# Optimization experiments

Measured on AMD Instinct MI355X. Metric: run time of the kernel, lower is better.

The kernel has to match this reference:

```python
import jax, jax.numpy as jnp
import numpy as np

B, L, D, H = 65536, 20, 4, 1024
T = 61  # output_length; 60 RK4 steps


def setup_inputs() -> dict:
    key = jax.random.key(0)
    ks = jax.random.split(key, 16)
    # small positive states so the quadratic SEIR dynamics stay finite over 60 steps
    xx = jax.random.uniform(ks[0], (B, L, D), dtype=jnp.float32) * 0.1
    dims = [L * D] + [H] * 6 + [3]
    inp = {"xx": xx}
    for i in range(7):
        scale = 1.0 / np.sqrt(dims[i])
        W = jax.random.normal(ks[1 + 2 * i], (dims[i], dims[i + 1]), dtype=jnp.float32) * scale
        if i == 6:
            W = W * 1e-3  # keep beta/gamma/sigma small -> stable integration
        inp[f"W{i}"] = W
        inp[f"b{i}"] = jnp.zeros((dims[i + 1],), jnp.float32)
    inp["output_length"] = T
    return inp


def reference(xx, W0, b0, W1, b1, W2, b2, W3, b3, W4, b4, W5, b5, W6, b6, output_length):
    h = xx.reshape(xx.shape[0], -1)  # (B, L*D)
    for W, b in ((W0, b0), (W1, b1), (W2, b2), (W3, b3), (W4, b4), (W5, b5)):
        h = jax.nn.leaky_relu(h @ W + b, negative_slope=0.01)
    out = h @ W6 + b6  # (B, 3)
    beta, gamma, sigma = out[:, 0:1], out[:, 1:2], out[:, 2:3]  # each (B,1)

    initial = xx[:, 0]  # (B, 4) = S,E,I,R at t0
    S0, E0, I0, R0 = (initial[:, i:i + 1] for i in range(4))
    # self.step = 1 in the torch module, so dt is folded in as 1.0

    def derivs(S, E, I):
        SI = beta * S * I
        return -SI, SI - sigma * E, sigma * E - gamma * I, gamma * I

    def body(carry, _):
        S, E, I, R = carry
        k1S, k1E, k1I, k1R = derivs(S, E, I)
        k2S, k2E, k2I, k2R = derivs(S + 0.5 * k1S, E + 0.5 * k1E, I + 0.5 * k1I)
        k3S, k3E, k3I, k3R = derivs(S + 0.5 * k2S, E + 0.5 * k2E, I + 0.5 * k2I)
        k4S, k4E, k4I, k4R = derivs(S + k3S, E + k3E, I + k3I)
        upd = lambda f, k1, k2, k3, k4: f + (k1 + 2 * k2 + 2 * k3 + k4) / 6.0
        new = (upd(S, k1S, k2S, k3S, k4S),
               upd(E, k1E, k2E, k3E, k4E),
               upd(I, k1I, k2I, k3I, k4I),
               upd(R, k1R, k2R, k3R, k4R))
        return new, jnp.concatenate(new, axis=1)  # (B,4) per step

    _, ys = jax.lax.scan(body, (S0, E0, I0, R0), None, length=output_length - 1)
    y0 = jnp.concatenate([S0, E0, I0, R0], axis=1)  # (B,4)
    y = jnp.concatenate([y0[None], ys], axis=0)     # (T,B,4)
    return jnp.transpose(y, (1, 0, 2))              # (B,T,4) in S,E,I,R order
```

## Files before the change

kernel.cpp:

```cpp
#include <hip/hip_runtime.h>
#include <stdint.h>

typedef short s16x8 __attribute__((ext_vector_type(8)));
typedef __bf16 bf16x8 __attribute__((ext_vector_type(8)));
typedef float f32x4 __attribute__((ext_vector_type(4)));

typedef const __attribute__((address_space(1))) void* gas_ptr;
typedef __attribute__((address_space(3))) void* las_ptr;

__device__ __forceinline__ unsigned short f2bf(float f) {
  unsigned u = __builtin_bit_cast(unsigned, f);
  u += 0x7FFFu + ((u >> 16) & 1u);
  return (unsigned short)(u >> 16);
}
__device__ __forceinline__ float bf2f(unsigned short h) {
  return __builtin_bit_cast(float, (unsigned)h << 16);
}

__device__ __forceinline__ void async16(const void* g, void* l) {
  __builtin_amdgcn_global_load_lds((gas_ptr)g, (las_ptr)l, 16, 0, 0);
}

__global__ void prep_x0(const float* __restrict__ xx, unsigned short* __restrict__ X0,
                        int rowOffset, int rows) {
  int idx = blockIdx.x * blockDim.x + threadIdx.x;
  if (idx >= rows * 128) return;
  int r = idx >> 7, c = idx & 127;
  float v = (c < 80) ? xx[(size_t)(rowOffset + r) * 80 + c] : 0.f;
  X0[(size_t)r * 128 + c] = f2bf(v);
}

__global__ void transpose_cast(const float* __restrict__ W, unsigned short* __restrict__ WT,
                               int K, int N, int KP) {
  __shared__ float tile[32][33];
  int n0 = blockIdx.x * 32, k0 = blockIdx.y * 32;
  int tx = threadIdx.x, ty = threadIdx.y;
  #pragma unroll
  for (int j = 0; j < 32; j += 8) {
    int k = k0 + ty + j;
    tile[ty + j][tx] = (k < K) ? W[(size_t)k * N + n0 + tx] : 0.f;
  }
  __syncthreads();
  #pragma unroll
  for (int j = 0; j < 32; j += 8) {
    WT[(size_t)(n0 + ty + j) * KP + k0 + tx] = f2bf(tile[tx][ty + j]);
  }
}

#define BM 128
#define BN 128
#define BK 64

__global__ void gemm_mlp(const unsigned short* __restrict__ A,
                         const unsigned short* __restrict__ BT,
                         const float* __restrict__ bias,
                         unsigned short* __restrict__ C,
                         int M, int N, int K, int leaky) {
  __shared__ unsigned short As[BM * BK];
  __shared__ unsigned short Bs[BN * BK];

  const int tid  = threadIdx.x;
  const int wid  = tid >> 6;
  const int lane = tid & 63;
  const int wr = (wid >> 1) * 64;
  const int wc = (wid & 1) * 64;
  const int bn = blockIdx.x * BN;
  const int bm = blockIdx.y * BM;

  const int srow = lane >> 3;
  const int scol = (lane & 7) * 8;

  f32x4 acc[4][4] = {};

  const unsigned short* aTile = A  + (size_t)bm * K;
  const unsigned short* bTile = BT + (size_t)bn * K;

  for (int k0 = 0; k0 < K; k0 += BK) {
    #pragma unroll
    for (int j = 0; j < 4; ++j) {
      const int rg = wid + j * 4;
      async16(aTile + (size_t)(rg * 8 + srow) * K + k0 + scol, &As[rg * 8 * BK]);
      async16(bTile + (size_t)(rg * 8 + srow) * K + k0 + scol, &Bs[rg * 8 * BK]);
    }
    __syncthreads();

    const int fr = lane & 15;
    const int kq = (lane >> 4) * 8;
    #pragma unroll
    for (int ks = 0; ks < BK; ks += 32) {
      const int kk = ks + kq;
      bf16x8 af[4], bv[4];
      #pragma unroll
      for (int m = 0; m < 4; ++m)
        af[m] = __builtin_bit_cast(bf16x8, *(const s16x8*)&As[(wr + m * 16 + fr) * BK + kk]);
      #pragma unroll
      for (int n = 0; n < 4; ++n)
        bv[n] = __builtin_bit_cast(bf16x8, *(const s16x8*)&Bs[(wc + n * 16 + fr) * BK + kk]);
      #pragma unroll
      for (int m = 0; m < 4; ++m)
        #pragma unroll
        for (int n = 0; n < 4; ++n)
          acc[m][n] = __builtin_amdgcn_mfma_f32_16x16x32_bf16(af[m], bv[n], acc[m][n], 0, 0, 0);
    }
    __syncthreads();
  }

  const int fcol = lane & 15;
  const int frow = (lane >> 4) * 4;
  #pragma unroll
  for (int m = 0; m < 4; ++m) {
    #pragma unroll
    for (int n = 0; n < 4; ++n) {
      const int col = bn + wc + n * 16 + fcol;
      const float bb = bias[col];
      #pragma unroll
      for (int r = 0; r < 4; ++r) {
        const int row = bm + wr + m * 16 + frow + r;
        float v = acc[m][n][r] + bb;
        if (leaky) v = (v > 0.f) ? v : 0.01f * v;
        C[(size_t)row * N + col] = f2bf(v);
      }
    }
  }
}

__global__ void head_gemv(const unsigned short* __restrict__ H,
                          const float* __restrict__ W6,
                          const float* __restrict__ b6,
                          float* __restrict__ bgs,
                          int rows) {
  const int w = (blockIdx.x * blockDim.x + threadIdx.x) >> 6;
  const int lane = threadIdx.x & 63;
  if (w >= rows) return;

  const unsigned short* h = H + (size_t)w * 1024 + lane * 16;
  float s0 = 0.f, s1 = 0.f, s2 = 0.f;
  #pragma unroll
  for (int i = 0; i < 16; i += 8) {
    s16x8 v = *(const s16x8*)(h + i);
    #pragma unroll
    for (int j = 0; j < 8; ++j) {
      const float hv = bf2f((unsigned short)v[j]);
      const int e = lane * 16 + i + j;
      s0 = fmaf(hv, W6[e * 3 + 0], s0);
      s1 = fmaf(hv, W6[e * 3 + 1], s1);
      s2 = fmaf(hv, W6[e * 3 + 2], s2);
    }
  }
  #pragma unroll
  for (int off = 1; off < 64; off <<= 1) {
    s0 += __shfl_xor(s0, off);
    s1 += __shfl_xor(s1, off);
    s2 += __shfl_xor(s2, off);
  }
  if (lane == 0) {
    float4 v = make_float4(s0 + b6[0], s1 + b6[1], s2 + b6[2], 0.f);
    *(float4*)(bgs + (size_t)w * 4) = v;
  }
}

__global__ void rk4_traj(const float* __restrict__ bgs,
                         const float* __restrict__ xx,
                         float* __restrict__ out,
                         int rowOffset, int rows, int T) {
  const int r = blockIdx.x * blockDim.x + threadIdx.x;
  if (r >= rows) return;
  const size_t grow = (size_t)rowOffset + r;

  const float4 bg = *(const float4*)(bgs + (size_t)r * 4);
  const float beta = bg.x, gamma = bg.y, sigma = bg.z;

  const float4 iv = *(const float4*)(xx + grow * 80);
  float S = iv.x, E = iv.y, I = iv.z, R = iv.w;
  float* o = out + grow * (size_t)T * 4;
  *(float4*)o = iv;

#define DERIVS(S_, E_, I_, dS, dE, dI, dR)      \
  {                                             \
    float SI = beta * (S_) * (I_);              \
    float sE = sigma * (E_);                    \
    float gI = gamma * (I_);                    \
    dS = -SI; dE = SI - sE; dI = sE - gI; dR = gI; \
  }

  for (int t = 1; t < T; ++t) {
    float k1S, k1E, k1I, k1R; DERIVS(S, E, I, k1S, k1E, k1I, k1R);
    float k2S, k2E, k2I, k2R; DERIVS(S + 0.5f * k1S, E + 0.5f * k1E, I + 0.5f * k1I, k2S, k2E, k2I, k2R);
    float k3S, k3E, k3I, k3R; DERIVS(S + 0.5f * k2S, E + 0.5f * k2E, I + 0.5f * k2I, k3S, k3E, k3I, k3R);
    float k4S, k4E, k4I, k4R; DERIVS(S + k3S, E + k3E, I + k3I, k4S, k4E, k4I, k4R);
    S += (k1S + 2.f * k2S + 2.f * k3S + k4S) * (1.f / 6.f);
    E += (k1E + 2.f * k2E + 2.f * k3E + k4E) * (1.f / 6.f);
    I += (k1I + 2.f * k2I + 2.f * k3I + k4I) * (1.f / 6.f);
    R += (k1R + 2.f * k2R + 2.f * k3R + k4R) * (1.f / 6.f);
    *(float4*)(o + (size_t)t * 4) = make_float4(S, E, I, R);
  }
#undef DERIVS
}

extern "C" void kernel_launch(void* const* d_in, const int* in_sizes, int n_in,
                              void* d_out, int out_size, void* d_ws, size_t ws_size,
                              hipStream_t stream) {
  const float* xx = (const float*)d_in[0];
  const float* W[7];
  const float* bb[7];
  for (int i = 0; i < 7; ++i) {
    W[i]  = (const float*)d_in[1 + 2 * i];
    bb[i] = (const float*)d_in[2 + 2 * i];
  }
  const int B = in_sizes[0] / 80;
  const int T = out_size / (B * 4);
  float* out = (float*)d_out;

  uint8_t* ws = (uint8_t*)d_ws;
  size_t off = 0;
  auto alloc = [&](size_t bytes) -> uint8_t* {
    uint8_t* p = ws + off;
    off += (bytes + 255) & ~(size_t)255;
    return p;
  };

  unsigned short* WTl[6];
  WTl[0] = (unsigned short*)alloc((size_t)1024 * 128 * 2);
  for (int i = 1; i < 6; ++i) WTl[i] = (unsigned short*)alloc((size_t)1024 * 1024 * 2);

  const size_t weightBytes = off;
  const size_t avail = ws_size > weightBytes ? ws_size - weightBytes : 0;
  int Bc = (int)(avail / 4368);
  Bc = (Bc / 128) * 128;
  if (Bc > B) Bc = B;
  if (Bc < 128) Bc = 128;

  unsigned short* X0   = (unsigned short*)alloc((size_t)Bc * 128 * 2);
  unsigned short* buf0 = (unsigned short*)alloc((size_t)Bc * 1024 * 2);
  unsigned short* buf1 = (unsigned short*)alloc((size_t)Bc * 1024 * 2);
  float* bgs           = (float*)alloc((size_t)Bc * 4 * 4);

  {
    dim3 blk(32, 8);
    transpose_cast<<<dim3(32, 4), blk, 0, stream>>>(W[0], WTl[0], 80, 1024, 128);
    for (int i = 1; i < 6; ++i)
      transpose_cast<<<dim3(32, 32), blk, 0, stream>>>(W[i], WTl[i], 1024, 1024, 1024);
  }

  for (int r0 = 0; r0 < B; r0 += Bc) {
    const int rows = (B - r0 < Bc) ? (B - r0) : Bc;

    {
      const int n = rows * 128;
      prep_x0<<<(n + 255) / 256, 256, 0, stream>>>(xx, X0, r0, rows);
    }

    const dim3 grid(8, rows / 128);
    gemm_mlp<<<grid, 256, 0, stream>>>(X0,   WTl[0], bb[0], buf0, rows, 1024, 128,  1);
    gemm_mlp<<<grid, 256, 0, stream>>>(buf0, WTl[1], bb[1], buf1, rows, 1024, 1024, 1);
    gemm_mlp<<<grid, 256, 0, stream>>>(buf1, WTl[2], bb[2], buf0, rows, 1024, 1024, 1);
    gemm_mlp<<<grid, 256, 0, stream>>>(buf0, WTl[3], bb[3], buf1, rows, 1024, 1024, 1);
    gemm_mlp<<<grid, 256, 0, stream>>>(buf1, WTl[4], bb[4], buf0, rows, 1024, 1024, 1);
    gemm_mlp<<<grid, 256, 0, stream>>>(buf0, WTl[5], bb[5], buf1, rows, 1024, 1024, 1);

    head_gemv<<<rows / 4, 256, 0, stream>>>(buf1, W[6], bb[6], bgs, rows);
    rk4_traj<<<(rows + 255) / 256, 256, 0, stream>>>(bgs, xx, out, r0, rows, T);
  }
}
```

Baseline: 1.123 ms.

## Add 256x256-tile 8-wave pipelined GEMM for the 1024x1024 MLP layers

Adds a new GEMM kernel using 256x256 output tiles, 512 threads and 128KB of dynamic LDS with double-buffered async global-to-LDS loads and XOR-swizzled layout. The K loop is split into four phases that interleave MFMA compute with staging of the next A/B halves, with barriers and s_setprio around the MFMA blocks. Workgroups are remapped across XCDs for locality. This targets higher arithmetic intensity and overlap of loads with compute in the five hidden 1024x1024 layers. The cost is heavy LDS and register use, which limits occupancy. Chunk rows are now rounded to multiples of 256.

```diff
diff --git a/kernel.cpp b/kernel.cpp
--- a/kernel.cpp
+++ b/kernel.cpp
@@ -118,6 +118,183 @@
         const int row = bm + wr + m * 16 + frow + r;
         float v = acc[m][n][r] + bb;
         if (leaky) v = (v > 0.f) ? v : 0.01f * v;
+        C[(size_t)row * N + col] = f2bf(v);
+      }
+    }
+  }
+}
+
+
+__device__ __forceinline__ void stage_half(const char* srcRow0, size_t ldb,
+                                           char* ldsHalf, int w, int rsub, int usw) {
+  #pragma unroll
+  for (int l = 0; l < 2; ++l) {
+    const char* src = srcRow0 + (size_t)((l * 8 + w) * 8 + rsub) * ldb + usw;
+    async16(src, ldsHalf + (l * 8 + w) * 1024);
+  }
+}
+
+#define MFMA16 __builtin_amdgcn_mfma_f32_16x16x32_bf16
+
+__global__ __launch_bounds__(512, 2)
+void gemm8(const unsigned short* __restrict__ A,
+           const unsigned short* __restrict__ BT,
+           const float* __restrict__ bias,
+           unsigned short* __restrict__ C,
+           int M, int N, int K) {
+  extern __shared__ char smem[];
+  char* smA = smem;
+  char* smB = smem + 65536;
+  const unsigned short* sA = (const unsigned short*)smA;
+  const unsigned short* sB = (const unsigned short*)smB;
+  const int NTk = K >> 6;
+
+  const int tid  = threadIdx.x;
+  const int w    = tid >> 6;
+  const int lane = tid & 63;
+
+  const int nwg = gridDim.x;
+  const int bid = blockIdx.x;
+  const int q = nwg >> 3, r = nwg & 7;
+  const int xcd = bid & 7, idx = bid >> 3;
+  const int wg = (xcd < r ? xcd * (q + 1) : r * (q + 1) + (xcd - r) * q) + idx;
+  const int nNT = N >> 8;
+  const int mtile = wg / nNT, ntile = wg % nNT;
+  const int bm = mtile << 8, bn = ntile << 8;
+
+  const int wr = (w >> 2) << 7;
+  const int wc = (w & 3) << 6;
+  const int fr = lane & 15;
+  const int e0 = lane >> 4;
+  const int sw = lane & 7;
+  const int rsub = lane >> 3;
+  const int usw  = ((sw ^ rsub) << 4);
+  const int col0 = (((e0)     ^ sw) << 3);
+  const int col1 = (((e0 + 4) ^ sw) << 3);
+
+  const size_t ldb = (size_t)K * 2;
+  const char* Ab = (const char*)A  + (size_t)bm * ldb;
+  const char* Bb = (const char*)BT + (size_t)bn * ldb;
+
+  f32x4 acc[8][4] = {};
+
+#define RDA(c_, row_, col_) __builtin_bit_cast(bf16x8, *(const s16x8*)&sA[(c_) * 16384 + (row_) * 64 + (col_)])
+#define RDB(c_, row_, col_) __builtin_bit_cast(bf16x8, *(const s16x8*)&sB[(c_) * 16384 + (row_) * 64 + (col_)])
+
+  stage_half(Bb,                    ldb, smB,                  w, rsub, usw);
+  stage_half(Bb + 128 * ldb,        ldb, smB + 16384,          w, rsub, usw);
+  stage_half(Ab,                    ldb, smA,                  w, rsub, usw);
+  stage_half(Ab + 128 * ldb,        ldb, smA + 16384,          w, rsub, usw);
+  stage_half(Bb + 128,              ldb, smB + 32768,          w, rsub, usw);
+  stage_half(Bb + 128 * ldb + 128,  ldb, smB + 32768 + 16384,  w, rsub, usw);
+  asm volatile("s_waitcnt vmcnt(4)" ::: "memory");
+  __builtin_amdgcn_s_barrier();
+
+  for (int kt = 0; kt < NTk; ++kt) {
+    const int c = kt & 1;
+    bf16x8 aF[4][2], bF[4][2];
+
+    #pragma unroll
+    for (int m = 0; m < 4; ++m) {
+      const int row = wr + m * 16 + fr;
+      aF[m][0] = RDA(c, row, col0);
+      aF[m][1] = RDA(c, row, col1);
+    }
+    #pragma unroll
+    for (int n = 0; n < 2; ++n) {
+      const int row = wc + n * 16 + fr;
+      bF[n][0] = RDB(c, row, col0);
+      bF[n][1] = RDB(c, row, col1);
+    }
+    if (kt + 1 < NTk)
+      stage_half(Ab + (size_t)(kt + 1) * 128, ldb, smA + (c ^ 1) * 32768, w, rsub, usw);
+    __builtin_amdgcn_s_barrier();
+    __builtin_amdgcn_s_setprio(1);
+    #pragma unroll
+    for (int m = 0; m < 4; ++m)
+      #pragma unroll
+      for (int n = 0; n < 2; ++n) {
+        acc[m][n] = MFMA16(aF[m][0], bF[n][0], acc[m][n], 0, 0, 0);
+        acc[m][n] = MFMA16(aF[m][1], bF[n][1], acc[m][n], 0, 0, 0);
+      }
+    __builtin_amdgcn_s_setprio(0);
+    __builtin_amdgcn_s_barrier();
+
+    #pragma unroll
+    for (int n = 2; n < 4; ++n) {
+      const int row = wc + n * 16 + fr;
+      bF[n][0] = RDB(c, row, col0);
+      bF[n][1] = RDB(c, row, col1);
+    }
+    if (kt + 1 < NTk)
+      stage_half(Ab + 128 * ldb + (size_t)(kt + 1) * 128, ldb,
+                 smA + (c ^ 1) * 32768 + 16384, w, rsub, usw);
+    __builtin_amdgcn_s_barrier();
+    __builtin_amdgcn_s_setprio(1);
+    #pragma unroll
+    for (int m = 0; m < 4; ++m)
+      #pragma unroll
+      for (int n = 2; n < 4; ++n) {
+        acc[m][n] = MFMA16(aF[m][0], bF[n][0], acc[m][n], 0, 0, 0);
+        acc[m][n] = MFMA16(aF[m][1], bF[n][1], acc[m][n], 0, 0, 0);
+      }
+    __builtin_amdgcn_s_setprio(0);
+    __builtin_amdgcn_s_barrier();
+
+    #pragma unroll
+    for (int m = 0; m < 4; ++m) {
+      const int row = wr + (m + 4) * 16 + fr;
+      aF[m][0] = RDA(c, row, col0);
+      aF[m][1] = RDA(c, row, col1);
+    }
+    if (kt + 2 < NTk)
+      stage_half(Bb + (size_t)(kt + 2) * 128, ldb, smB + c * 32768, w, rsub, usw);
+    __builtin_amdgcn_s_barrier();
+    __builtin_amdgcn_s_setprio(1);
+    #pragma unroll
+    for (int m = 0; m < 4; ++m)
+      #pragma unroll
+      for (int n = 0; n < 2; ++n) {
+        acc[m + 4][n] = MFMA16(aF[m][0], bF[n][0], acc[m + 4][n], 0, 0, 0);
+        acc[m + 4][n] = MFMA16(aF[m][1], bF[n][1], acc[m + 4][n], 0, 0, 0);
+      }
+    __builtin_amdgcn_s_setprio(0);
+    __builtin_amdgcn_s_barrier();
+
+    if (kt + 2 < NTk)
+      stage_half(Bb + 128 * ldb + (size_t)(kt + 2) * 128, ldb,
+                 smB + c * 32768 + 16384, w, rsub, usw);
+    __builtin_amdgcn_s_barrier();
+    __builtin_amdgcn_s_setprio(1);
+    #pragma unroll
+    for (int m = 0; m < 4; ++m)
+      #pragma unroll
+      for (int n = 2; n < 4; ++n) {
+        acc[m + 4][n] = MFMA16(aF[m][0], bF[n][0], acc[m + 4][n], 0, 0, 0);
+        acc[m + 4][n] = MFMA16(aF[m][1], bF[n][1], acc[m + 4][n], 0, 0, 0);
+      }
+    __builtin_amdgcn_s_setprio(0);
+    if (kt + 2 < NTk) asm volatile("s_waitcnt vmcnt(4)" ::: "memory");
+    else              asm volatile("s_waitcnt vmcnt(0)" ::: "memory");
+    __builtin_amdgcn_s_barrier();
+  }
+
+#undef RDA
+#undef RDB
+
+  const int fcol = lane & 15;
+  const int frow = e0 << 2;
+  #pragma unroll
+  for (int n = 0; n < 4; ++n) {
+    const int col = bn + wc + n * 16 + fcol;
+    const float bb = bias[col];
+    #pragma unroll
+    for (int m = 0; m < 8; ++m) {
+      #pragma unroll
+      for (int rr = 0; rr < 4; ++rr) {
+        const int row = bm + wr + m * 16 + frow + rr;
+        float v = acc[m][n][rr] + bb;
+        v = (v > 0.f) ? v : 0.01f * v;
         C[(size_t)row * N + col] = f2bf(v);
       }
     }
@@ -211,6 +388,9 @@
   const int T = out_size / (B * 4);
   float* out = (float*)d_out;
 
+  hipFuncSetAttribute((const void*)gemm8,
+                      hipFuncAttributeMaxDynamicSharedMemorySize, 131072);
+
   uint8_t* ws = (uint8_t*)d_ws;
   size_t off = 0;
   auto alloc = [&](size_t bytes) -> uint8_t* {
@@ -226,9 +406,9 @@
   const size_t weightBytes = off;
   const size_t avail = ws_size > weightBytes ? ws_size - weightBytes : 0;
   int Bc = (int)(avail / 4368);
-  Bc = (Bc / 128) * 128;
+  Bc = (Bc / 256) * 256;
   if (Bc > B) Bc = B;
-  if (Bc < 128) Bc = 128;
+  if (Bc < 256) Bc = 256;
 
   unsigned short* X0   = (unsigned short*)alloc((size_t)Bc * 128 * 2);
   unsigned short* buf0 = (unsigned short*)alloc((size_t)Bc * 1024 * 2);
@@ -250,13 +430,15 @@
       prep_x0<<<(n + 255) / 256, 256, 0, stream>>>(xx, X0, r0, rows);
     }
 
-    const dim3 grid(8, rows / 128);
-    gemm_mlp<<<grid, 256, 0, stream>>>(X0,   WTl[0], bb[0], buf0, rows, 1024, 128,  1);
-    gemm_mlp<<<grid, 256, 0, stream>>>(buf0, WTl[1], bb[1], buf1, rows, 1024, 1024, 1);
-    gemm_mlp<<<grid, 256, 0, stream>>>(buf1, WTl[2], bb[2], buf0, rows, 1024, 1024, 1);
-    gemm_mlp<<<grid, 256, 0, stream>>>(buf0, WTl[3], bb[3], buf1, rows, 1024, 1024, 1);
-    gemm_mlp<<<grid, 256, 0, stream>>>(buf1, WTl[4], bb[4], buf0, rows, 1024, 1024, 1);
-    gemm_mlp<<<grid, 256, 0, stream>>>(buf0, WTl[5], bb[5], buf1, rows, 1024, 1024, 1);
+    gemm_mlp<<<dim3(8, rows / 128), 256, 0, stream>>>(X0, WTl[0], bb[0], buf0,
+                                                      rows, 1024, 128, 1);
+
+    const int nwg = (rows / 256) * 4;
+    gemm8<<<nwg, 512, 131072, stream>>>(buf0, WTl[1], bb[1], buf1, rows, 1024, 1024);
+    gemm8<<<nwg, 512, 131072, stream>>>(buf1, WTl[2], bb[2], buf0, rows, 1024, 1024);
+    gemm8<<<nwg, 512, 131072, stream>>>(buf0, WTl[3], bb[3], buf1, rows, 1024, 1024);
+    gemm8<<<nwg, 512, 131072, stream>>>(buf1, WTl[4], bb[4], buf0, rows, 1024, 1024);
+    gemm8<<<nwg, 512, 131072, stream>>>(buf0, WTl[5], bb[5], buf1, rows, 1024, 1024);
 
     head_gemv<<<rows / 4, 256, 0, stream>>>(buf1, W[6], bb[6], bgs, rows);
     rk4_traj<<<(rows + 255) / 256, 256, 0, stream>>>(bgs, xx, out, r0, rows, T);
```

Measured after the change: 1.096 ms. 2.4% less time.
